# Kernel tuning notes

Measured on AMD Instinct MI355X. Metric: run time of the kernel, lower is better.

## Reference

```python
import jax, jax.numpy as jnp
import numpy as np
from jax import lax

DECAY = 0.1
THRESH = 0.5
LENS = 1.0
D_IN = 2 * 34 * 34  # 2312
HID = 800
NC = 10

@jax.custom_vjp
def act_fun(x):
    return (x > THRESH).astype(x.dtype)

def _act_fwd(x):
    return act_fun(x), x

def _act_bwd(x, g):
    p = jax.nn.sigmoid((x - THRESH) / LENS)
    return (g * p * (1.0 - p) / LENS,)

act_fun.defvjp(_act_fwd, _act_bwd)


def setup_inputs() -> dict:
    key = jax.random.key(0)
    ks = jax.random.split(key, 8)
    B, T = 128, 300
    inp = jax.random.uniform(ks[0], (B, 2, 34, 34, 50), dtype=jnp.float32)
    X = jnp.zeros((B, 2, 34, 34, T), dtype=jnp.float32)
    idx = jax.random.randint(ks[1], (B,), 0, T - 50)
    W1 = jax.random.normal(ks[2], (HID, D_IN), dtype=jnp.float32) * 0.02
    b1 = jnp.zeros((HID,), dtype=jnp.float32)
    W2 = jax.random.normal(ks[3], (NC, HID), dtype=jnp.float32) * 0.03
    b2 = jnp.zeros((NC,), dtype=jnp.float32)
    Wc = jax.random.uniform(ks[4], (1, HID + 4), dtype=jnp.float32)  # ctrl init U(0,1)
    bc = jax.random.uniform(ks[5], (1,), dtype=jnp.float32)
    return {"input": inp, "X": X, "idx": idx, "W1": W1, "b1": b1,
            "W2": W2, "b2": b2, "Wc": Wc, "bc": bc}


def _paste(Xi, clip_i, idx_i):
    # X[i, :, :, :, idx:idx+50] = input[i].view(2,34,34,50)
    return lax.dynamic_update_slice(Xi, clip_i, (0, 0, 0, idx_i))


def reference(input, X, idx, W1, b1, W2, b2, Wc, bc):
    B = X.shape[0]
    T = X.shape[-1]
    X = jax.vmap(_paste)(X, input, idx.astype(jnp.int32))
    xs = jnp.moveaxis(X.reshape(B, D_IN, T), -1, 0)  # [T, B, D_IN]

    t = jnp.arange(T)
    freqs = jnp.stack([
        jnp.ones(T), (t % 2 == 0).astype(jnp.float32),
        (t % 10 == 0).astype(jnp.float32), (t % 100 == 0).astype(jnp.float32),
    ], axis=1).astype(X.dtype)  # [T, 4]
    is_first = (t == 0)

    f32 = X.dtype
    carry0 = (
        jnp.zeros((B, HID), f32), jnp.zeros((B, HID), f32),   # h1_mem, h1_spike
        jnp.zeros((B, NC), f32), jnp.zeros((B, NC), f32),     # h2_mem, h2_spike
        jnp.zeros((B, 1), f32), jnp.zeros((B, 1), f32),       # c_mem, c_spike
        jnp.ones((B, 1), f32), jnp.zeros((B, NC), f32),       # bgt, h2_sumspike
    )

    def step(carry, inps):
        h1m, h1s, h2m, h2s, cm, cs, bgt, sum2 = carry
        x, fq, first = inps
        x_a = jnp.where(first, x, x * cs)
        bgt = jnp.where(cs == 1.0, bgt + 1.0, bgt)
        h1m = h1m * DECAY * (1.0 - h1s) + x_a @ W1.T + b1
        h1s = act_fun(h1m)
        h2m = h2m * DECAY * (1.0 - h2s) + h1s @ W2.T + b2
        h2s = act_fun(h2m)
        c_in = jnp.concatenate(
            [lax.stop_gradient(h1s), jnp.broadcast_to(fq, (B, 4))], axis=1)
        cm = cm * 0.1 * (1.0 - cs) + c_in @ Wc.T + bc
        cs = act_fun(cm)
        sum2 = sum2 + h2s
        return (h1m, h1s, h2m, h2s, cm, cs, bgt, sum2), None

    carry, _ = lax.scan(step, carry0, (xs, freqs, is_first))
    bgt, sum2 = carry[6], carry[7]
    rate = sum2 / bgt
    return rate, X
```

## Files before the change

### kernel.cpp

```cpp
#include <hip/hip_runtime.h>

#define D_IN 2312
#define HID  800
#define NCLS 10
#define BATCH 128
#define TSTEPS 300
#define WIN  50

#define MT 32
#define NT 32
#define BKK 16
#define NTILES_M 200
#define NTILES_N 25
#define GEMM_BLOCKS (NTILES_M * NTILES_N)
#define PASTE_BLOCKS 4096
#define TOTQ (BATCH * D_IN * (TSTEPS / 4))

__global__ __launch_bounds__(64) void fused_kernel(
    const float* __restrict__ inp,
    const float* __restrict__ W1,
    const int*   __restrict__ idx,
    float*       __restrict__ P,
    float*       __restrict__ outX)
{
  __shared__ float As[BKK][MT];
  __shared__ float Bs[BKK][NT + 4];

  int l  = threadIdx.x;
  int bx = blockIdx.x;

  if (bx < GEMM_BLOCKS) {
    int nt = bx / NTILES_M;
    int mt = bx - nt * NTILES_M;
    int m0 = mt * MT, n0 = nt * NT;

    int am = l & 31;
    int ak = l >> 5;
    int r  = m0 + am;
    int bb = r / 50, ss = r - bb * 50;
    const float* aptr = inp + (size_t)bb * (D_IN * WIN) + ss;

    int bn = l >> 4;
    int bk = l & 15;

    int lm = l & 7;
    int ln = l >> 3;
    int tm = lm * 4, tn = ln * 4;

    float aN[8], bN[8];
#pragma unroll
    for (int q = 0; q < 8; ++q) aN[q] = aptr[(ak * 8 + q) * WIN];
#pragma unroll
    for (int p = 0; p < 8; ++p)
      bN[p] = W1[(size_t)(n0 + bn + 4 * p) * D_IN + bk];

    float acc[4][4] = {};

    for (int k0 = 0; k0 < D_IN; k0 += BKK) {
#pragma unroll
      for (int q = 0; q < 8; ++q) As[ak * 8 + q][am] = aN[q];
#pragma unroll
      for (int p = 0; p < 8; ++p) Bs[bk][bn + 4 * p] = bN[p];
      __syncthreads();

      int kn0 = k0 + BKK;
      if (kn0 < D_IN) {
#pragma unroll
        for (int q = 0; q < 8; ++q) {
          int kk = kn0 + ak * 8 + q;
          aN[q] = (kk < D_IN) ? aptr[kk * WIN] : 0.f;
        }
#pragma unroll
        for (int p = 0; p < 8; ++p) {
          int kk = kn0 + bk;
          bN[p] = (kk < D_IN) ? W1[(size_t)(n0 + bn + 4 * p) * D_IN + kk] : 0.f;
        }
      }

#pragma unroll
      for (int kk = 0; kk < BKK; ++kk) {
        float4 A0 = *(const float4*)&As[kk][tm];
        float4 B0 = *(const float4*)&Bs[kk][tn];
        float av[4] = {A0.x, A0.y, A0.z, A0.w};
        float bv[4] = {B0.x, B0.y, B0.z, B0.w};
#pragma unroll
        for (int i = 0; i < 4; ++i)
#pragma unroll
          for (int j = 0; j < 4; ++j)
            acc[i][j] += av[i] * bv[j];
      }
      __syncthreads();
    }

#pragma unroll
    for (int i = 0; i < 4; ++i) {
      int row = m0 + tm + i;
      *(float4*)&P[(size_t)row * HID + n0 + tn] =
          make_float4(acc[i][0], acc[i][1], acc[i][2], acc[i][3]);
    }
  } else {
    int tid = (bx - GEMM_BLOCKS) * 64 + l;
    const int stride = PASTE_BLOCKS * 64;
    for (int i = tid; i < TOTQ; i += stride) {
      int q  = i % 75;
      int rd = i / 75;
      int b  = rd / D_IN;
      int d  = rd - b * D_IN;
      int ib = idx[b];
      const float* ip = inp + (size_t)b * (D_IN * WIN) + (size_t)d * WIN;
      int t0 = q * 4;
      float v[4];
#pragma unroll
      for (int e = 0; e < 4; ++e) {
        unsigned w = (unsigned)(t0 + e - ib);
        v[e] = (w < (unsigned)WIN) ? ip[w] : 0.f;
      }
      *(float4*)&outX[(size_t)rd * TSTEPS + t0] = make_float4(v[0], v[1], v[2], v[3]);
    }
  }
}

__global__ __launch_bounds__(64) void recur_kernel(
    const float* __restrict__ P,
    const float* __restrict__ W2,
    const float* __restrict__ b2,
    const float* __restrict__ Wc,
    const float* __restrict__ bc,
    const float* __restrict__ b1,
    const int*   __restrict__ idx,
    float*       __restrict__ out)
{
  __shared__ float sW2row[NCLS][832];
  __shared__ float sWc[832];
  __shared__ unsigned short sM[TSTEPS][64];
  __shared__ int sSteps[TSTEPS];

  int L = threadIdx.x;
  int b = blockIdx.x;

#pragma unroll
  for (int c = 0; c < NCLS; ++c)
    for (int base = 0; base < 832; base += 64) {
      int j = base + L;
      sW2row[c][j] = (j < HID) ? W2[c * HID + j] : 0.f;
    }
  for (int base = 0; base < 832; base += 64) {
    int j = base + L;
    sWc[j] = (j < HID) ? Wc[j] : 0.f;
  }

  int myidx = idx[b];
  const float* Pb = P + (size_t)b * WIN * HID;

  float m[13], b1r[13];
  unsigned smask = 0;
#pragma unroll
  for (int rr = 0; rr < 13; ++rr) {
    int j = L + 64 * rr;
    m[rr] = 0.f;
    b1r[rr] = (j < HID) ? b1[j] : 0.f;
  }

  float cm = 0.f, cs = 0.f, bgt = 1.f;
  float bc0 = bc[0];
  float wf0 = Wc[HID], wf1 = Wc[HID + 1], wf2 = Wc[HID + 2], wf3 = Wc[HID + 3];
  int cnt = 0;

  __syncthreads();

  for (int step = 0; step < TSTEPS; ++step) {
    float gate = (step == 0) ? 1.f : cs;
    unsigned w = (unsigned)(step - myidx);
    float cur[13];
    if (w < (unsigned)WIN && gate != 0.f) {
      const float* Pr = Pb + (size_t)w * HID;
#pragma unroll
      for (int rr = 0; rr < 13; ++rr) {
        int j = L + 64 * rr;
        cur[rr] = (j < HID) ? Pr[j] : 0.f;
      }
    } else {
#pragma unroll
      for (int rr = 0; rr < 13; ++rr) cur[rr] = 0.f;
    }

    unsigned nmask = 0;
#pragma unroll
    for (int rr = 0; rr < 13; ++rr) {
      float mprev = ((smask >> rr) & 1u) ? 0.f : m[rr] * 0.1f;
      float mv = mprev + cur[rr] * gate + b1r[rr];
      m[rr] = mv;
      nmask |= (mv > 0.5f) ? (1u << rr) : 0u;
    }
    smask = nmask;

    unsigned long long ball = __ballot(smask != 0u);

    float ctrl = 0.f;
    if (ball) {
      float cacc = 0.f;
#pragma unroll
      for (int rr = 0; rr < 13; ++rr) {
        float f = (float)((smask >> rr) & 1u);
        cacc = fmaf(f, sWc[L + 64 * rr], cacc);
      }
      cacc += __shfl_xor(cacc, 1);
      cacc += __shfl_xor(cacc, 2);
      cacc += __shfl_xor(cacc, 4);
      cacc += __shfl_xor(cacc, 8);
      cacc += __shfl_xor(cacc, 16);
      cacc += __shfl_xor(cacc, 32);
      ctrl = cacc;

      sM[cnt][L] = (unsigned short)smask;
      if (L == 0) sSteps[cnt] = step;
      ++cnt;
    }

    bgt += (cs == 1.f) ? 1.f : 0.f;
    float fq = wf0;
    if ((step & 1) == 0)   fq += wf1;
    if (step % 10 == 0)    fq += wf2;
    if (step % 100 == 0)   fq += wf3;
    float cv = (cs != 0.f ? 0.f : cm * 0.1f) + ctrl + fq + bc0;
    cm = cv;
    cs = (cv > 0.5f) ? 1.f : 0.f;
  }

  float h2m[10], h2s[10], sum2[10], b2r[10];
#pragma unroll
  for (int c = 0; c < NCLS; ++c) { h2m[c] = 0.f; h2s[c] = 0.f; sum2[c] = 0.f; b2r[c] = b2[c]; }

  int ptr = 0;
  for (int t = 0; t < TSTEPS; ++t) {
    float dot[10];
#pragma unroll
    for (int c = 0; c < NCLS; ++c) dot[c] = 0.f;

    if (ptr < cnt && sSteps[ptr] == t) {
      unsigned msk = (unsigned)sM[ptr][L];
#pragma unroll
      for (int rr = 0; rr < 13; ++rr) {
        float f = (float)((msk >> rr) & 1u);
        int j = L + 64 * rr;
#pragma unroll
        for (int c = 0; c < NCLS; ++c)
          dot[c] = fmaf(f, sW2row[c][j], dot[c]);
      }
#pragma unroll
      for (int c = 0; c < NCLS; ++c) {
        float v = dot[c];
        v += __shfl_xor(v, 1);
        v += __shfl_xor(v, 2);
        v += __shfl_xor(v, 4);
        v += __shfl_xor(v, 8);
        v += __shfl_xor(v, 16);
        v += __shfl_xor(v, 32);
        dot[c] = v;
      }
      ++ptr;
    }

#pragma unroll
    for (int c = 0; c < NCLS; ++c) {
      float v = (h2s[c] != 0.f ? 0.f : h2m[c] * 0.1f) + dot[c] + b2r[c];
      h2m[c] = v;
      h2s[c] = (v > 0.5f) ? 1.f : 0.f;
      sum2[c] += h2s[c];
    }
  }

  if (L == 0) {
#pragma unroll
    for (int c = 0; c < NCLS; ++c) out[b * NCLS + c] = sum2[c] / bgt;
  }
}

extern "C" void kernel_launch(void* const* d_in, const int* in_sizes, int n_in,
                              void* d_out, int out_size, void* d_ws, size_t ws_size,
                              hipStream_t stream) {
  const float* inp = (const float*)d_in[0];
  const int*   idx = (const int*)d_in[2];
  const float* W1  = (const float*)d_in[3];
  const float* b1  = (const float*)d_in[4];
  const float* W2  = (const float*)d_in[5];
  const float* b2  = (const float*)d_in[6];
  const float* Wc  = (const float*)d_in[7];
  const float* bc  = (const float*)d_in[8];

  float* out = (float*)d_out;
  float* P   = (float*)d_ws;

  fused_kernel<<<GEMM_BLOCKS + PASTE_BLOCKS, 64, 0, stream>>>(
      inp, W1, idx, P, out + BATCH * NCLS);

  recur_kernel<<<BATCH, 64, 0, stream>>>(P, W2, b2, Wc, bc, b1, idx, out);
}
```

Baseline: 1.214 ms.

## Enlarge GEMM tiles, prefetch next P row, and merge recurrence loops

The fused GEMM+paste kernel moves to 128-thread blocks with 64-row M tiles, halving the GEMM and paste block counts. The recurrent kernel now prefetches the next timestep's P row one iteration ahead, keeps Wc in registers instead of LDS, and folds the layer-2 spike update into the main time loop instead of recording masks for a second pass. This removes LDS mask buffers and one serial 300-step loop, in exchange for higher register pressure and always loading P rows even when the gate is zero.

Measured after the change: 1.123 ms. -7.5%, faster.

```diff
diff --git a/kernel.cpp b/kernel.cpp
--- a/kernel.cpp
+++ b/kernel.cpp
@@ -7,16 +7,17 @@
 #define TSTEPS 300
 #define WIN  50
 
-#define MT 32
+#define MT 64
 #define NT 32
 #define BKK 16
-#define NTILES_M 200
-#define NTILES_N 25
-#define GEMM_BLOCKS (NTILES_M * NTILES_N)
-#define PASTE_BLOCKS 4096
+#define NTM 100
+#define NTN 25
+#define GEMM_BLOCKS (NTM * NTN)
+#define PASTE_BLOCKS 2048
+#define BLK 128
 #define TOTQ (BATCH * D_IN * (TSTEPS / 4))
 
-__global__ __launch_bounds__(64) void fused_kernel(
+__global__ __launch_bounds__(BLK) void fused_kernel(
     const float* __restrict__ inp,
     const float* __restrict__ W1,
     const int*   __restrict__ idx,
@@ -26,54 +27,56 @@
   __shared__ float As[BKK][MT];
   __shared__ float Bs[BKK][NT + 4];
 
-  int l  = threadIdx.x;
+  int t  = threadIdx.x;
   int bx = blockIdx.x;
 
   if (bx < GEMM_BLOCKS) {
-    int nt = bx / NTILES_M;
-    int mt = bx - nt * NTILES_M;
+    int nt = bx / NTM;
+    int mt = bx - nt * NTM;
     int m0 = mt * MT, n0 = nt * NT;
 
-    int am = l & 31;
-    int ak = l >> 5;
+    int am = t & 63;
+    int ah = t >> 6;
     int r  = m0 + am;
     int bb = r / 50, ss = r - bb * 50;
     const float* aptr = inp + (size_t)bb * (D_IN * WIN) + ss;
 
-    int bn = l >> 4;
-    int bk = l & 15;
-
+    int bn = t >> 4;
+    int bk = t & 15;
+
+    int l  = t & 63;
     int lm = l & 7;
     int ln = l >> 3;
-    int tm = lm * 4, tn = ln * 4;
-
-    float aN[8], bN[8];
-#pragma unroll
-    for (int q = 0; q < 8; ++q) aN[q] = aptr[(ak * 8 + q) * WIN];
-#pragma unroll
-    for (int p = 0; p < 8; ++p)
-      bN[p] = W1[(size_t)(n0 + bn + 4 * p) * D_IN + bk];
+    int tm = ah * 32 + lm * 4;
+    int tn = ln * 4;
+
+    float aN[8], bN[4];
+#pragma unroll
+    for (int q = 0; q < 8; ++q) aN[q] = aptr[(ah * 8 + q) * WIN];
+#pragma unroll
+    for (int p = 0; p < 4; ++p)
+      bN[p] = W1[(size_t)(n0 + bn + 8 * p) * D_IN + bk];
 
     float acc[4][4] = {};
 
     for (int k0 = 0; k0 < D_IN; k0 += BKK) {
 #pragma unroll
-      for (int q = 0; q < 8; ++q) As[ak * 8 + q][am] = aN[q];
-#pragma unroll
-      for (int p = 0; p < 8; ++p) Bs[bk][bn + 4 * p] = bN[p];
+      for (int q = 0; q < 8; ++q) As[ah * 8 + q][am] = aN[q];
+#pragma unroll
+      for (int p = 0; p < 4; ++p) Bs[bk][bn + 8 * p] = bN[p];
       __syncthreads();
 
       int kn0 = k0 + BKK;
       if (kn0 < D_IN) {
 #pragma unroll
         for (int q = 0; q < 8; ++q) {
-          int kk = kn0 + ak * 8 + q;
+          int kk = kn0 + ah * 8 + q;
           aN[q] = (kk < D_IN) ? aptr[kk * WIN] : 0.f;
         }
 #pragma unroll
-        for (int p = 0; p < 8; ++p) {
+        for (int p = 0; p < 4; ++p) {
           int kk = kn0 + bk;
-          bN[p] = (kk < D_IN) ? W1[(size_t)(n0 + bn + 4 * p) * D_IN + kk] : 0.f;
+          bN[p] = (kk < D_IN) ? W1[(size_t)(n0 + bn + 8 * p) * D_IN + kk] : 0.f;
         }
       }
 
@@ -99,8 +102,8 @@
           make_float4(acc[i][0], acc[i][1], acc[i][2], acc[i][3]);
     }
   } else {
-    int tid = (bx - GEMM_BLOCKS) * 64 + l;
-    const int stride = PASTE_BLOCKS * 64;
+    int tid = (bx - GEMM_BLOCKS) * BLK + t;
+    const int stride = PASTE_BLOCKS * BLK;
     for (int i = tid; i < TOTQ; i += stride) {
       int q  = i % 75;
       int rd = i / 75;
@@ -120,7 +123,7 @@
   }
 }
 
-__global__ __launch_bounds__(64) void recur_kernel(
+__global__ __launch_bounds__(64, 1) void recur_kernel(
     const float* __restrict__ P,
     const float* __restrict__ W2,
     const float* __restrict__ b2,
@@ -131,9 +134,6 @@
     float*       __restrict__ out)
 {
   __shared__ float sW2row[NCLS][832];
-  __shared__ float sWc[832];
-  __shared__ unsigned short sM[TSTEPS][64];
-  __shared__ int sSteps[TSTEPS];
 
   int L = threadIdx.x;
   int b = blockIdx.x;
@@ -144,36 +144,35 @@
       int j = base + L;
       sW2row[c][j] = (j < HID) ? W2[c * HID + j] : 0.f;
     }
-  for (int base = 0; base < 832; base += 64) {
-    int j = base + L;
-    sWc[j] = (j < HID) ? Wc[j] : 0.f;
-  }
 
   int myidx = idx[b];
   const float* Pb = P + (size_t)b * WIN * HID;
 
-  float m[13], b1r[13];
+  float m[13], b1r[13], wcr[13];
   unsigned smask = 0;
 #pragma unroll
   for (int rr = 0; rr < 13; ++rr) {
     int j = L + 64 * rr;
-    m[rr] = 0.f;
+    m[rr]   = 0.f;
     b1r[rr] = (j < HID) ? b1[j] : 0.f;
+    wcr[rr] = (j < HID) ? Wc[j] : 0.f;
   }
 
   float cm = 0.f, cs = 0.f, bgt = 1.f;
   float bc0 = bc[0];
   float wf0 = Wc[HID], wf1 = Wc[HID + 1], wf2 = Wc[HID + 2], wf3 = Wc[HID + 3];
-  int cnt = 0;
+
+  float h2m[10], h2s[10], sum2[10], b2r[10];
+#pragma unroll
+  for (int c = 0; c < NCLS; ++c) { h2m[c] = 0.f; h2s[c] = 0.f; sum2[c] = 0.f; b2r[c] = b2[c]; }
 
   __syncthreads();
 
-  for (int step = 0; step < TSTEPS; ++step) {
-    float gate = (step == 0) ? 1.f : cs;
-    unsigned w = (unsigned)(step - myidx);
-    float cur[13];
-    if (w < (unsigned)WIN && gate != 0.f) {
-      const float* Pr = Pb + (size_t)w * HID;
+  float cur[13];
+  {
+    unsigned w0 = (unsigned)(0 - myidx);
+    if (w0 < (unsigned)WIN) {
+      const float* Pr = Pb + (size_t)w0 * HID;
 #pragma unroll
       for (int rr = 0; rr < 13; ++rr) {
         int j = L + 64 * rr;
@@ -182,6 +181,26 @@
     } else {
 #pragma unroll
       for (int rr = 0; rr < 13; ++rr) cur[rr] = 0.f;
+    }
+  }
+
+  for (int step = 0; step < TSTEPS; ++step) {
+    float gate = (step == 0) ? 1.f : cs;
+
+    float nxt[13];
+    {
+      unsigned wn = (unsigned)(step + 1 - myidx);
+      if (wn < (unsigned)WIN) {
+        const float* Pr = Pb + (size_t)wn * HID;
+#pragma unroll
+        for (int rr = 0; rr < 13; ++rr) {
+          int j = L + 64 * rr;
+          nxt[rr] = (j < HID) ? Pr[j] : 0.f;
+        }
+      } else {
+#pragma unroll
+        for (int rr = 0; rr < 13; ++rr) nxt[rr] = 0.f;
+      }
     }
 
     unsigned nmask = 0;
@@ -197,12 +216,16 @@
     unsigned long long ball = __ballot(smask != 0u);
 
     float ctrl = 0.f;
+    float dot[10];
+#pragma unroll
+    for (int c = 0; c < NCLS; ++c) dot[c] = 0.f;
+
     if (ball) {
       float cacc = 0.f;
 #pragma unroll
       for (int rr = 0; rr < 13; ++rr) {
         float f = (float)((smask >> rr) & 1u);
-        cacc = fmaf(f, sWc[L + 64 * rr], cacc);
+        cacc = fmaf(f, wcr[rr], cacc);
       }
       cacc += __shfl_xor(cacc, 1);
       cacc += __shfl_xor(cacc, 2);
@@ -212,36 +235,9 @@
       cacc += __shfl_xor(cacc, 32);
       ctrl = cacc;
 
-      sM[cnt][L] = (unsigned short)smask;
-      if (L == 0) sSteps[cnt] = step;
-      ++cnt;
-    }
-
-    bgt += (cs == 1.f) ? 1.f : 0.f;
-    float fq = wf0;
-    if ((step & 1) == 0)   fq += wf1;
-    if (step % 10 == 0)    fq += wf2;
-    if (step % 100 == 0)   fq += wf3;
-    float cv = (cs != 0.f ? 0.f : cm * 0.1f) + ctrl + fq + bc0;
-    cm = cv;
-    cs = (cv > 0.5f) ? 1.f : 0.f;
-  }
-
-  float h2m[10], h2s[10], sum2[10], b2r[10];
-#pragma unroll
-  for (int c = 0; c < NCLS; ++c) { h2m[c] = 0.f; h2s[c] = 0.f; sum2[c] = 0.f; b2r[c] = b2[c]; }
-
-  int ptr = 0;
-  for (int t = 0; t < TSTEPS; ++t) {
-    float dot[10];
-#pragma unroll
-    for (int c = 0; c < NCLS; ++c) dot[c] = 0.f;
-
-    if (ptr < cnt && sSteps[ptr] == t) {
-      unsigned msk = (unsigned)sM[ptr][L];
 #pragma unroll
       for (int rr = 0; rr < 13; ++rr) {
-        float f = (float)((msk >> rr) & 1u);
+        float f = (float)((smask >> rr) & 1u);
         int j = L + 64 * rr;
 #pragma unroll
         for (int c = 0; c < NCLS; ++c)
@@ -258,8 +254,16 @@
         v += __shfl_xor(v, 32);
         dot[c] = v;
       }
-      ++ptr;
-    }
+    }
+
+    bgt += (cs == 1.f) ? 1.f : 0.f;
+    float fq = wf0;
+    if ((step & 1) == 0)   fq += wf1;
+    if (step % 10 == 0)    fq += wf2;
+    if (step % 100 == 0)   fq += wf3;
+    float cv = (cs != 0.f ? 0.f : cm * 0.1f) + ctrl + fq + bc0;
+    cm = cv;
+    cs = (cv > 0.5f) ? 1.f : 0.f;
 
 #pragma unroll
     for (int c = 0; c < NCLS; ++c) {
@@ -268,6 +272,9 @@
       h2s[c] = (v > 0.5f) ? 1.f : 0.f;
       sum2[c] += h2s[c];
     }
+
+#pragma unroll
+    for (int rr = 0; rr < 13; ++rr) cur[rr] = nxt[rr];
   }
 
   if (L == 0) {
@@ -291,7 +298,7 @@
   float* out = (float*)d_out;
   float* P   = (float*)d_ws;
 
-  fused_kernel<<<GEMM_BLOCKS + PASTE_BLOCKS, 64, 0, stream>>>(
+  fused_kernel<<<GEMM_BLOCKS + PASTE_BLOCKS, BLK, 0, stream>>>(
       inp, W1, idx, P, out + BATCH * NCLS);
 
   recur_kernel<<<BATCH, 64, 0, stream>>>(P, W2, b2, Wc, bc, b1, idx, out);
```
